# Performance work log

Measured on AMD Instinct MI355X. Metric: run time of the kernel, lower is better.

The kernel has to match this reference:

```python
import jax, jax.numpy as jnp
import numpy as np
import math

B, N, C, H = 32, 512, 768, 12
HD = C // H
KEEP_RATE = 0.7
SCALE = HD ** -0.5
BOUNDARY = math.ceil(KEEP_RATE * (N - 1))  # 358


def setup_inputs() -> dict:
    key = jax.random.key(0)
    k1, k2, k3, k4 = jax.random.split(key, 4)
    x = jax.random.normal(k1, (B, N, C), jnp.float32) * 0.02
    # prefix (left-aligned) key-padding mask: valid length per sample in [N//4, N]
    lengths = jax.random.randint(k2, (B,), N // 4, N + 1)
    key_mask = (jnp.arange(N)[None, :] < lengths[:, None])  # [B, N]
    attn_mask = jnp.broadcast_to(key_mask[:, None, :], (B, N, N)).astype(jnp.int32)
    w_qkv = jax.random.normal(k3, (C, 3 * C), jnp.float32) * (C ** -0.5)
    w_proj = jax.random.normal(k4, (C, C), jnp.float32) * (C ** -0.5)
    b_proj = jnp.zeros((C,), jnp.float32)
    return {"x": x, "attn_mask": attn_mask, "w_qkv": w_qkv, "w_proj": w_proj, "b_proj": b_proj}


def reference(x, attn_mask, w_qkv, w_proj, b_proj):
    # qkv projection and head split: [B,N,3C] -> [3,B,H,N,HD]
    qkv = (x @ w_qkv).reshape(B, N, 3, H, HD).transpose(2, 0, 3, 1, 4)
    q, k, v = qkv[0], qkv[1], qkv[2]
    attn = jnp.einsum('bhqd,bhkd->bhqk', q, k) * SCALE          # [B,H,N,N]
    mask4 = attn_mask[:, None, :, :]                            # broadcast over heads
    attn = jnp.where(mask4 == 0, jnp.float32(-1e9), attn)
    attn = jax.nn.softmax(attn, axis=-1)
    out = jnp.einsum('bhqk,bhkd->bhqd', attn, v)                # [B,H,N,HD]
    out = out.transpose(0, 2, 1, 3).reshape(B, N, C)
    out = out @ w_proj + b_proj

    # per-sample top-k token pruning based on CLS attention (keep_rate < 1)
    key_row = attn_mask[:, 0, 1:]                               # [B, N-1] key padding row
    cls_mean = attn[:, :, 0, 1:].mean(axis=1)                   # mean over heads, [B, N-1]
    valid = key_row != 0
    scores = jnp.where(valid, cls_mean, -jnp.inf)
    valid_count = valid.sum(axis=1)                             # [B]
    left = jnp.ceil(valid_count.astype(jnp.float32) * KEEP_RATE).astype(jnp.int32)
    _, top_idx = jax.lax.top_k(scores, BOUNDARY)                # sorted desc, [B, BOUNDARY]
    pos = jnp.arange(BOUNDARY)[None, :]
    # slots beyond per-sample left_tokens are padded with 1e9 (matches torch cat padding)
    idx = jnp.where(pos < left[:, None], top_idx.astype(jnp.float32), jnp.float32(1e9))
    index = jnp.broadcast_to(idx[:, :, None], (B, BOUNDARY, C))
    return (out, index, idx, BOUNDARY)
```

## Files before the change

### kernel.cpp

```cpp
#include <hip/hip_runtime.h>
#include <hip/hip_bf16.h>

#define Bb 32
#define Nn 512
#define Cc 768
#define Hh 12
#define HDd 64
#define BND 358
#define QS 0.18033688f

typedef unsigned short u16;
typedef unsigned int u32;
typedef __attribute__((ext_vector_type(8))) short bf16x8;
typedef __attribute__((ext_vector_type(4))) float f32x4;
typedef __attribute__((ext_vector_type(16))) float f32x16;
typedef __attribute__((ext_vector_type(4))) int i32x4;

__device__ __forceinline__ f32x4 MFMA16(bf16x8 a, bf16x8 b, f32x4 c) {
  return __builtin_amdgcn_mfma_f32_16x16x32_bf16(a, b, c, 0, 0, 0);
}
__device__ __forceinline__ f32x16 MFMA32(bf16x8 a, bf16x8 b, f32x16 c) {
  return __builtin_amdgcn_mfma_f32_32x32x16_bf16(a, b, c, 0, 0, 0);
}

__device__ __forceinline__ float fexp2(float x) { return __builtin_amdgcn_exp2f(x); }

__device__ __forceinline__ u32 f2bf(float f) {
  u32 u = __builtin_bit_cast(u32, f);
  return (u + 0x7fffu + ((u >> 16) & 1u)) >> 16;
}
__device__ __forceinline__ u32 packbf2(float a, float b) { return f2bf(a) | (f2bf(b) << 16); }
__device__ __forceinline__ u32 cvtpk2(float a, float b) {
  float2 f2 = {a, b};
  __hip_bfloat162 h = __float22bfloat162_rn(f2);
  u32 r;
  __builtin_memcpy(&r, &h, 4);
  return r;
}
__device__ __forceinline__ float bf2f(u16 h) { return __builtin_bit_cast(float, (u32)h << 16); }

__device__ __forceinline__ void async_copy16(void* lds, const void* g) {
  __builtin_amdgcn_global_load_lds((const __attribute__((address_space(1))) void*)g,
                                   (__attribute__((address_space(3))) void*)lds, 16, 0, 0);
}


__global__ __launch_bounds__(256) void k_convx(const float* __restrict__ x, u16* __restrict__ xb) {
  int gid = blockIdx.x * 256 + threadIdx.x;
  if (gid >= (Bb * Nn * Cc) / 4) return;
  float4 v = *(const float4*)&x[gid * 4];
  u32 p0 = packbf2(v.x, v.y), p1 = packbf2(v.z, v.w);
  uint2 st = {p0, p1};
  *(uint2*)&xb[gid * 4] = st;
}

__global__ __launch_bounds__(256) void k_transpose(const float* __restrict__ src, u16* __restrict__ dst,
                                                   int R, int Ccols) {
  __shared__ float tbuf[32][33];
  int c0 = blockIdx.x * 32, r0 = blockIdx.y * 32;
  int lx = threadIdx.x & 31, ly = threadIdx.x >> 5;
  #pragma unroll
  for (int rr = ly; rr < 32; rr += 8) tbuf[rr][lx] = src[(long)(r0 + rr) * Ccols + c0 + lx];
  __syncthreads();
  #pragma unroll
  for (int cc = ly; cc < 32; cc += 8) dst[(long)(c0 + cc) * R + r0 + lx] = (u16)f2bf(tbuf[lx][cc]);
}

__global__ __launch_bounds__(256) void k_lens(const int* __restrict__ mask, int* __restrict__ lens) {
  int b = blockIdx.x, t = threadIdx.x;
  __shared__ int red[256];
  red[t] = mask[(long)b * Nn * Nn + t] + mask[(long)b * Nn * Nn + t + 256];
  __syncthreads();
  for (int s = 128; s > 0; s >>= 1) {
    if (t < s) red[t] += red[t + s];
    __syncthreads();
  }
  if (t == 0) lens[b] = red[0];
}

__global__ __launch_bounds__(64) void k_order(const int* __restrict__ lens, int* __restrict__ ord) {
  __shared__ int ls[32];
  int t = threadIdx.x;
  if (t < 32) ls[t] = lens[t];
  __syncthreads();
  if (t < 32) {
    int mylen = ls[t];
    int rank = 0;
    #pragma unroll
    for (int j = 0; j < 32; ++j) {
      int lj = ls[j];
      rank += (lj > mylen || (lj == mylen && j < t)) ? 1 : 0;
    }
    int s = (rank < 16) ? (2 * rank) : (2 * (31 - rank) + 1);
    ord[s] = t;
  }
}

template <int MODE, int SWAP>
__global__ __launch_bounds__(256) void k_gemm2(const u16* __restrict__ A, const u16* __restrict__ Bt,
                                               int nb0, u16* __restrict__ Qo, u16* __restrict__ Ko,
                                               u16* __restrict__ Vto, float* __restrict__ Co,
                                               const float* __restrict__ bias) {
  __shared__ u16 As[2][128 * 64];
  __shared__ u16 Bs[2][128 * 64];
  int m0 = blockIdx.x * 128;
  int nb = nb0 + blockIdx.y * 128;
  int t = threadIdx.x, lane = t & 63, wave = t >> 6;
  int wr = wave >> 1, wc = wave & 1;
  int qlane = lane & 15, g = lane >> 4;
  f32x4 acc[4][4] = {};

  auto stage = [&](int kt, int buf) {
    #pragma unroll
    for (int i = 0; i < 4; ++i) {
      int chunk = i * 256 + t;
      int row = chunk >> 3;
      int cp = (chunk & 7) << 4;
      int src = cp ^ ((row & 7) << 4);
      const u16* ga = A + (long)(m0 + row) * 768 + kt * 64 + (src >> 1);
      const u16* gb = Bt + (long)(nb + row) * 768 + kt * 64 + (src >> 1);
      async_copy16(&As[buf][(i * 256 + wave * 64) * 8], ga);
      async_copy16(&Bs[buf][(i * 256 + wave * 64) * 8], gb);
    }
  };

  auto compute = [&](int buf) {
    #pragma unroll
    for (int kk = 0; kk < 2; ++kk) {
      bf16x8 af[4], bf[4];
      #pragma unroll
      for (int x = 0; x < 4; ++x) {
        int ra = wr * 64 + x * 16 + qlane;
        int ca = (kk * 64 + g * 16) ^ ((ra & 7) << 4);
        af[x] = *(const bf16x8*)&As[buf][ra * 64 + (ca >> 1)];
        int rb = wc * 64 + x * 16 + qlane;
        int cb = (kk * 64 + g * 16) ^ ((rb & 7) << 4);
        bf[x] = *(const bf16x8*)&Bs[buf][rb * 64 + (cb >> 1)];
      }
      #pragma unroll
      for (int mi = 0; mi < 4; ++mi)
        #pragma unroll
        for (int ni = 0; ni < 4; ++ni)
          acc[mi][ni] = SWAP ? MFMA16(bf[ni], af[mi], acc[mi][ni])
                             : MFMA16(af[mi], bf[ni], acc[mi][ni]);
    }
  };

  stage(0, 0);
  __syncthreads();
  int cur = 0;
  for (int kt = 0; kt < 12; ++kt) {
    if (kt < 11) stage(kt + 1, cur ^ 1);
    compute(cur);
    __syncthreads();
    cur ^= 1;
  }

  if (MODE == 0 && SWAP == 1) {
    #pragma unroll
    for (int mi = 0; mi < 4; ++mi) {
      int m = m0 + wr * 64 + mi * 16 + qlane;
      int b = m >> 9, qi = m & 511;
      #pragma unroll
      for (int ni = 0; ni < 4; ++ni) {
        int nf = nb + wc * 64 + ni * 16 + g * 4;
        int which = nf >= 768;
        int rem = nf - which * 768;
        int hh = rem >> 6, d0 = rem & 63;
        u16* dst = (which ? Ko : Qo) + ((long)(b * Hh + hh) * Nn + qi) * HDd + d0;
        float sc = which ? 1.f : QS;
        uint2 st = {packbf2(acc[mi][ni][0] * sc, acc[mi][ni][1] * sc),
                    packbf2(acc[mi][ni][2] * sc, acc[mi][ni][3] * sc)};
        *(uint2*)dst = st;
      }
    }
  } else if (MODE == 0) {
    #pragma unroll
    for (int mi = 0; mi < 4; ++mi) {
      int m = m0 + wr * 64 + mi * 16 + g * 4;
      int b = m >> 9, qi = m & 511;
      #pragma unroll
      for (int ni = 0; ni < 4; ++ni) {
        int rem = nb + wc * 64 + ni * 16 + qlane - 1536;
        int hh = rem >> 6, d = rem & 63;
        u16* dst = Vto + (long)(b * Hh + hh) * (Nn * HDd) + (qi >> 5) * 2048 + d * 32 + (qi & 31);
        uint2 st = {packbf2(acc[mi][ni][0], acc[mi][ni][1]),
                    packbf2(acc[mi][ni][2], acc[mi][ni][3])};
        *(uint2*)dst = st;
      }
    }
  } else {
    #pragma unroll
    for (int mi = 0; mi < 4; ++mi) {
      int m = m0 + wr * 64 + mi * 16 + qlane;
      #pragma unroll
      for (int ni = 0; ni < 4; ++ni) {
        int n0 = nb + wc * 64 + ni * 16 + g * 4;
        float4 bv = *(const float4*)&bias[n0];
        float4 st = {acc[mi][ni][0] + bv.x, acc[mi][ni][1] + bv.y,
                     acc[mi][ni][2] + bv.z, acc[mi][ni][3] + bv.w};
        *(float4*)&Co[(long)m * Cc + n0] = st;
      }
    }
  }
}

__global__ __launch_bounds__(64) void k_attn(const u16* __restrict__ Q, const u16* __restrict__ K,
                                             const u16* __restrict__ Vt, const int* __restrict__ lens,
                                             const int* __restrict__ ord, u16* __restrict__ AO) {
  int lane = threadIdx.x;
  int bid = blockIdx.x;
  int bh = bid % (Bb * Hh);
  int chunk = bid / (Bb * Hh);
  int b = ord[bh / Hh];
  int h = bh % Hh;
  int q0w = chunk * 64;
  int ln = lane & 31, hi = lane >> 5;
  int len = lens[b];
  int nt = (len + 31) >> 5;

  const u16* Qb = Q + (long)(b * Hh + h) * Nn * HDd;
  const u16* Kb = K + (long)(b * Hh + h) * Nn * HDd;
  const u16* Vb = Vt + (long)(b * Hh + h) * Nn * HDd;

  bf16x8 qf[2][4];
  #pragma unroll
  for (int qt = 0; qt < 2; ++qt)
    #pragma unroll
    for (int ds = 0; ds < 4; ++ds)
      qf[qt][ds] = *(const bf16x8*)(Qb + (q0w + qt * 32 + ln) * HDd + ds * 16 + hi * 8);

  f32x16 o[2][2] = {};
  float l[2] = {0.f, 0.f};

  auto loadt = [&](bf16x8 (&kf)[4], bf16x8 (&vf)[2][2], int t) {
    int k0 = t * 32;
    #pragma unroll
    for (int ds = 0; ds < 4; ++ds)
      kf[ds] = *(const bf16x8*)(Kb + (k0 + ln) * HDd + ds * 16 + hi * 8);
    #pragma unroll
    for (int dt = 0; dt < 2; ++dt)
      #pragma unroll
      for (int ks = 0; ks < 2; ++ks)
        vf[dt][ks] = *(const bf16x8*)(Vb + t * 2048 + (dt * 32 + ln) * 32 + ks * 16 + hi * 8);
  };

  auto compute = [&](const bf16x8 (&kf)[4], const bf16x8 (&vf)[2][2], int t) {
    int k0 = t * 32;
    bool bdry = (k0 + 32 > len);
    int khi = k0 + 4 * hi;
    #pragma unroll
    for (int qt = 0; qt < 2; ++qt) {
      f32x16 st = {};
      #pragma unroll
      for (int ds = 0; ds < 4; ++ds) st = MFMA32(kf[ds], qf[qt][ds], st);
      if (bdry) {
        #pragma unroll
        for (int r = 0; r < 16; ++r) {
          int key = khi + (r & 3) + 8 * (r >> 2);
          if (key >= len) st[r] = -1e9f;
        }
      }
      float p[16];
      #pragma unroll
      for (int r = 0; r < 16; ++r) p[r] = fexp2(st[r]);
      l[qt] += (((p[0] + p[1]) + (p[2] + p[3])) + ((p[4] + p[5]) + (p[6] + p[7]))) +
               (((p[8] + p[9]) + (p[10] + p[11])) + ((p[12] + p[13]) + (p[14] + p[15])));
      u32 wA0 = cvtpk2(p[0], p[1]), wA1 = cvtpk2(p[2], p[3]);
      u32 wA2 = cvtpk2(p[4], p[5]), wA3 = cvtpk2(p[6], p[7]);
      asm volatile("v_permlane32_swap_b32 %0, %1" : "+v"(wA0), "+v"(wA2));
      asm volatile("v_permlane32_swap_b32 %0, %1" : "+v"(wA1), "+v"(wA3));
      u32 wB0 = cvtpk2(p[8], p[9]), wB1 = cvtpk2(p[10], p[11]);
      u32 wB2 = cvtpk2(p[12], p[13]), wB3 = cvtpk2(p[14], p[15]);
      asm volatile("v_permlane32_swap_b32 %0, %1" : "+v"(wB0), "+v"(wB2));
      asm volatile("v_permlane32_swap_b32 %0, %1" : "+v"(wB1), "+v"(wB3));
      i32x4 bi0 = {(int)wA0, (int)wA1, (int)wA2, (int)wA3};
      i32x4 bi1 = {(int)wB0, (int)wB1, (int)wB2, (int)wB3};
      bf16x8 pb0 = __builtin_bit_cast(bf16x8, bi0);
      bf16x8 pb1 = __builtin_bit_cast(bf16x8, bi1);
      #pragma unroll
      for (int dt = 0; dt < 2; ++dt) {
        o[qt][dt] = MFMA32(vf[dt][0], pb0, o[qt][dt]);
        o[qt][dt] = MFMA32(vf[dt][1], pb1, o[qt][dt]);
      }
    }
  };

  bf16x8 kfA[4], vfA[2][2], kfB[4], vfB[2][2];
  loadt(kfA, vfA, 0);
  int t = 0;
  #pragma unroll 1
  for (; t + 2 <= nt; t += 2) {
    loadt(kfB, vfB, t + 1);
    compute(kfA, vfA, t);
    if (t + 2 < nt) loadt(kfA, vfA, t + 2);
    compute(kfB, vfB, t + 1);
  }
  if (t < nt) compute(kfA, vfA, t);

  #pragma unroll
  for (int qt = 0; qt < 2; ++qt) {
    float ls = l[qt] + __shfl_xor(l[qt], 32);
    float inv = 1.f / ls;
    u16* outp = AO + ((long)(b * Nn + q0w + qt * 32 + ln) * Cc) + h * HDd;
    #pragma unroll
    for (int dt = 0; dt < 2; ++dt) {
      #pragma unroll
      for (int qd = 0; qd < 4; ++qd) {
        uint2 st2 = {cvtpk2(o[qt][dt][4 * qd + 0] * inv, o[qt][dt][4 * qd + 1] * inv),
                     cvtpk2(o[qt][dt][4 * qd + 2] * inv, o[qt][dt][4 * qd + 3] * inv)};
        *(uint2*)(outp + dt * 32 + 8 * qd + 4 * hi) = st2;
      }
    }
  }
}

__global__ __launch_bounds__(256) void k_sco_init(float* __restrict__ sco) {
  int gid = blockIdx.x * 256 + threadIdx.x;
  if (gid < Bb * 511) sco[gid] = 0.f;
}

__global__ __launch_bounds__(256) void k_cls(const u16* __restrict__ Q, const u16* __restrict__ K,
                                             const int* __restrict__ lens, float* __restrict__ scores) {
  int bh = blockIdx.x;
  int b = bh / Hh;
  int t = threadIdx.x;
  int len = lens[b];
  __shared__ float qrow[64];
  __shared__ float red[256];
  const u16* Qb = Q + (long)bh * Nn * HDd;
  const u16* Kb = K + (long)bh * Nn * HDd;
  if (t < 64) qrow[t] = bf2f(Qb[t]);
  __syncthreads();
  const bf16x8* kr0 = (const bf16x8*)(Kb + t * HDd);
  const bf16x8* kr1 = (const bf16x8*)(Kb + (t + 256) * HDd);
  float d0 = 0.f, d1 = 0.f;
  #pragma unroll
  for (int c8 = 0; c8 < 8; ++c8) {
    bf16x8 kv0 = kr0[c8], kv1 = kr1[c8];
    #pragma unroll
    for (int j = 0; j < 8; ++j) {
      float qv = qrow[c8 * 8 + j];
      d0 += qv * bf2f((u16)kv0[j]);
      d1 += qv * bf2f((u16)kv1[j]);
    }
  }
  float l0 = (t < len) ? d0 : -1e9f;
  float l1 = (t + 256 < len) ? d1 : -1e9f;
  red[t] = fmaxf(l0, l1);
  __syncthreads();
  for (int ss = 128; ss > 0; ss >>= 1) {
    if (t < ss) red[t] = fmaxf(red[t], red[t + ss]);
    __syncthreads();
  }
  float mx = red[0];
  __syncthreads();
  float e0 = fexp2(l0 - mx), e1 = fexp2(l1 - mx);
  red[t] = e0 + e1;
  __syncthreads();
  for (int ss = 128; ss > 0; ss >>= 1) {
    if (t < ss) red[t] += red[t + ss];
    __syncthreads();
  }
  float w = (1.f / 12.f) / red[0];
  if (t >= 1) atomicAdd(&scores[b * 511 + (t - 1)], e0 * w);
  atomicAdd(&scores[b * 511 + (t + 255)], e1 * w);
}

__device__ __forceinline__ bool sless(float sa, int ia, float sb, int ib) {
  return (sa > sb) || (sa == sb && ia < ib);
}

__global__ __launch_bounds__(256) void k_topk(const float* __restrict__ scores,
                                              const int* __restrict__ lens, float* __restrict__ dout) {
  int b = blockIdx.x, t = threadIdx.x;
  __shared__ float sc[512];
  __shared__ int id[512];
  float ninf = -__builtin_inff();
  int len = lens[b];
  for (int i = t; i < 512; i += 256) {
    sc[i] = (i < 511 && (i + 1) < len) ? scores[b * 511 + i] : ninf;
    id[i] = i;
  }
  for (int k = 2; k <= 512; k <<= 1) {
    for (int j = k >> 1; j > 0; j >>= 1) {
      __syncthreads();
      for (int i = t; i < 512; i += 256) {
        int ixj = i ^ j;
        if (ixj > i) {
          float si = sc[i], sj = sc[ixj];
          int ii = id[i], ij = id[ixj];
          bool up = ((i & k) == 0);
          bool dosw = up ? sless(sj, ij, si, ii) : sless(si, ii, sj, ij);
          if (dosw) {
            sc[i] = sj; sc[ixj] = si;
            id[i] = ij; id[ixj] = ii;
          }
        }
      }
    }
  }
  __syncthreads();
  int left = (int)ceilf((float)(len - 1) * 0.7f);
  const long OFF_IDX = (long)Bb * Nn * Cc + (long)Bb * BND * Cc;
  for (int p = t; p < BND; p += 256) {
    dout[OFF_IDX + (long)b * BND + p] = (p < left) ? (float)id[p] : 1e9f;
  }
  if (b == 0 && t == 0) dout[OFF_IDX + (long)Bb * BND] = (float)BND;
}

__global__ __launch_bounds__(256) void k_bcast(float* __restrict__ dout) {
  long gid = (long)blockIdx.x * 256 + threadIdx.x;
  const long total = (long)Bb * BND * (Cc / 4);
  if (gid >= total) return;
  long bp = gid / (Cc / 4);
  int c4 = (int)(gid % (Cc / 4));
  const long OFF_INDEX = (long)Bb * Nn * Cc;
  const long OFF_IDX = OFF_INDEX + (long)Bb * BND * Cc;
  float v = dout[OFF_IDX + bp];
  float4 f = {v, v, v, v};
  *(float4*)&dout[OFF_INDEX + bp * Cc + (long)c4 * 4] = f;
}

extern "C" void kernel_launch(void* const* d_in, const int* in_sizes, int n_in,
                              void* d_out, int out_size, void* d_ws, size_t ws_size,
                              hipStream_t stream) {
  const float* x = (const float*)d_in[0];
  const int* mask = (const int*)d_in[1];
  const float* wqkv = (const float*)d_in[2];
  const float* wproj = (const float*)d_in[3];
  const float* bproj = (const float*)d_in[4];
  float* out = (float*)d_out;

  char* ws = (char*)d_ws;
  u16* Qw  = (u16*)(ws);
  u16* Kw  = (u16*)(ws + 25165824L);
  u16* Vtw = (u16*)(ws + 50331648L);
  u16* XB  = (u16*)(ws + 75497472L);
  u16* AO  = XB;
  u16* WQT = (u16*)(ws + 100663296L);
  u16* WPT = (u16*)(ws + 104202240L);
  float* SCO = (float*)(ws + 105381888L);
  int* LEN = (int*)(ws + 105447424L);
  int* ORD = (int*)(ws + 105447552L);

  k_convx<<<12288, 256, 0, stream>>>(x, XB);
  k_transpose<<<dim3(72, 24), 256, 0, stream>>>(wqkv, WQT, 768, 2304);
  k_transpose<<<dim3(24, 24), 256, 0, stream>>>(wproj, WPT, 768, 768);
  k_lens<<<32, 256, 0, stream>>>(mask, LEN);
  k_order<<<1, 64, 0, stream>>>(LEN, ORD);
  k_sco_init<<<64, 256, 0, stream>>>(SCO);
  k_gemm2<0, 1><<<dim3(128, 12), 256, 0, stream>>>(XB, WQT, 0, Qw, Kw, nullptr, nullptr, nullptr);
  k_gemm2<0, 0><<<dim3(128, 6), 256, 0, stream>>>(XB, WQT, 1536, nullptr, nullptr, Vtw, nullptr, nullptr);
  k_attn<<<3072, 64, 0, stream>>>(Qw, Kw, Vtw, LEN, ORD, AO);
  k_gemm2<1, 1><<<dim3(128, 6), 256, 0, stream>>>(AO, WPT, 0, nullptr, nullptr, nullptr, out, bproj);
  k_cls<<<384, 256, 0, stream>>>(Qw, Kw, LEN, SCO);
  k_topk<<<32, 256, 0, stream>>>(SCO, LEN, out);
  k_bcast<<<8592, 256, 0, stream>>>(out);
}
```

Baseline: 226.1 us.

## Add 4-stage async-copy pipelined GEMM kernel for Q/K projection

Measured after the change: 238.6 us. +5.6%, slower.

```diff
diff --git a/kernel.cpp b/kernel.cpp
--- a/kernel.cpp
+++ b/kernel.cpp
@@ -93,6 +93,88 @@
     }
     int s = (rank < 16) ? (2 * rank) : (2 * (31 - rank) + 1);
     ord[s] = t;
+  }
+}
+
+__global__ __launch_bounds__(256) void k_gemmqk(const u16* __restrict__ A, const u16* __restrict__ Bt,
+                                                u16* __restrict__ Qo, u16* __restrict__ Ko) {
+  __shared__ u16 As[4][64 * 64];
+  __shared__ u16 Bs[4][64 * 64];
+  int m0 = blockIdx.x * 128;
+  int nb = blockIdx.y * 128;
+  int t = threadIdx.x, lane = t & 63, wave = t >> 6;
+  int wr = wave >> 1, wc = wave & 1;
+  int qlane = lane & 15, g = lane >> 4;
+  f32x4 acc[4][4] = {};
+
+  auto stage = [&](int kt, int buf) {
+    #pragma unroll
+    for (int i = 0; i < 2; ++i) {
+      int c = i * 256 + t;
+      int p = c >> 3;
+      int w = (c & 7) << 4;
+      int wl = w ^ ((p & 7) << 4);
+      int m = 2 * p + (wl >> 6);
+      int ke = (wl & 63) >> 1;
+      const u16* ga = A + (long)(m0 + m) * 768 + kt * 32 + ke;
+      const u16* gb = Bt + (long)(nb + m) * 768 + kt * 32 + ke;
+      async_copy16(&As[buf][(i * 256 + wave * 64) * 8], ga);
+      async_copy16(&Bs[buf][(i * 256 + wave * 64) * 8], gb);
+    }
+  };
+
+  auto compute = [&](int buf) {
+    bf16x8 af[4], bf[4];
+    #pragma unroll
+    for (int x = 0; x < 4; ++x) {
+      int ma = wr * 64 + x * 16 + qlane;
+      int pa = ma >> 1;
+      int wa = (((ma & 1) << 6) + (g << 4)) ^ ((pa & 7) << 4);
+      af[x] = *(const bf16x8*)((const char*)&As[buf][0] + pa * 128 + wa);
+      int mb = wc * 64 + x * 16 + qlane;
+      int pb = mb >> 1;
+      int wb = (((mb & 1) << 6) + (g << 4)) ^ ((pb & 7) << 4);
+      bf[x] = *(const bf16x8*)((const char*)&Bs[buf][0] + pb * 128 + wb);
+    }
+    #pragma unroll
+    for (int mi = 0; mi < 4; ++mi)
+      #pragma unroll
+      for (int ni = 0; ni < 4; ++ni)
+        acc[mi][ni] = MFMA16(bf[ni], af[mi], acc[mi][ni]);
+  };
+
+  stage(0, 0);
+  stage(1, 1);
+  stage(2, 2);
+  #pragma unroll 1
+  for (int kt = 0; kt < 24; ++kt) {
+    if (kt < 22)
+      asm volatile("s_waitcnt vmcnt(8)" ::: "memory");
+    else if (kt == 22)
+      asm volatile("s_waitcnt vmcnt(4)" ::: "memory");
+    else
+      asm volatile("s_waitcnt vmcnt(0)" ::: "memory");
+    __builtin_amdgcn_s_barrier();
+    if (kt + 3 < 24) stage(kt + 3, (kt + 3) & 3);
+    compute(kt & 3);
+  }
+
+  #pragma unroll
+  for (int mi = 0; mi < 4; ++mi) {
+    int m = m0 + wr * 64 + mi * 16 + qlane;
+    int b = m >> 9, qi = m & 511;
+    #pragma unroll
+    for (int ni = 0; ni < 4; ++ni) {
+      int nf = nb + wc * 64 + ni * 16 + g * 4;
+      int which = nf >= 768;
+      int rem = nf - which * 768;
+      int hh = rem >> 6, d0 = rem & 63;
+      u16* dst = (which ? Ko : Qo) + ((long)(b * Hh + hh) * Nn + qi) * HDd + d0;
+      float sc = which ? 1.f : QS;
+      uint2 st = {packbf2(acc[mi][ni][0] * sc, acc[mi][ni][1] * sc),
+                  packbf2(acc[mi][ni][2] * sc, acc[mi][ni][3] * sc)};
+      *(uint2*)dst = st;
+    }
   }
 }
 
@@ -156,25 +238,7 @@
     cur ^= 1;
   }
 
-  if (MODE == 0 && SWAP == 1) {
-    #pragma unroll
-    for (int mi = 0; mi < 4; ++mi) {
-      int m = m0 + wr * 64 + mi * 16 + qlane;
-      int b = m >> 9, qi = m & 511;
-      #pragma unroll
-      for (int ni = 0; ni < 4; ++ni) {
-        int nf = nb + wc * 64 + ni * 16 + g * 4;
-        int which = nf >= 768;
-        int rem = nf - which * 768;
-        int hh = rem >> 6, d0 = rem & 63;
-        u16* dst = (which ? Ko : Qo) + ((long)(b * Hh + hh) * Nn + qi) * HDd + d0;
-        float sc = which ? 1.f : QS;
-        uint2 st = {packbf2(acc[mi][ni][0] * sc, acc[mi][ni][1] * sc),
-                    packbf2(acc[mi][ni][2] * sc, acc[mi][ni][3] * sc)};
-        *(uint2*)dst = st;
-      }
-    }
-  } else if (MODE == 0) {
+  if (MODE == 0) {
     #pragma unroll
     for (int mi = 0; mi < 4; ++mi) {
       int m = m0 + wr * 64 + mi * 16 + g * 4;
@@ -450,7 +514,7 @@
   k_lens<<<32, 256, 0, stream>>>(mask, LEN);
   k_order<<<1, 64, 0, stream>>>(LEN, ORD);
   k_sco_init<<<64, 256, 0, stream>>>(SCO);
-  k_gemm2<0, 1><<<dim3(128, 12), 256, 0, stream>>>(XB, WQT, 0, Qw, Kw, nullptr, nullptr, nullptr);
+  k_gemmqk<<<dim3(128, 12), 256, 0, stream>>>(XB, WQT, Qw, Kw);
   k_gemm2<0, 0><<<dim3(128, 6), 256, 0, stream>>>(XB, WQT, 1536, nullptr, nullptr, Vtw, nullptr, nullptr);
   k_attn<<<3072, 64, 0, stream>>>(Qw, Kw, Vtw, LEN, ORD, AO);
   k_gemm2<1, 1><<<dim3(128, 6), 256, 0, stream>>>(AO, WPT, 0, nullptr, nullptr, nullptr, out, bproj);
```
